# Kernel tuning notes

Measured on AMD Instinct MI355X. Metric: run time of the kernel, lower is better.

## Reference

```python
import jax, jax.numpy as jnp
import numpy as np
from jax import lax

B, T, F0 = 16, 1024, 128
L_CNN, L_RNN, D = 3, 3, 512
NF = F0 // 2  # 64, freq dim after stride-2 conv
EPS = 1e-5


def conv2d(x, w, b, stride, pad):
    # x: [B,C,H,W], w: [O,I,kh,kw]
    y = lax.conv_general_dilated(x, w, (stride, stride), [(pad, pad), (pad, pad)],
                                 dimension_numbers=('NCHW', 'OIHW', 'NCHW'))
    return y + b[None, :, None, None]


def ln_last(x, g, b):
    m = x.mean(-1, keepdims=True)
    v = ((x - m) ** 2).mean(-1, keepdims=True)
    return (x - m) * lax.rsqrt(v + EPS) * g + b


def ln_feats(x, g, b):
    # LayerNorm over freq axis (axis 2) of [B,C,F,T] (== transpose(2,3); LN; transpose back)
    m = x.mean(2, keepdims=True)
    v = ((x - m) ** 2).mean(2, keepdims=True)
    return (x - m) * lax.rsqrt(v + EPS) * g[None, None, :, None] + b[None, None, :, None]


def sru_dir(u, x_res, v, b, reverse):
    # u: [T,B,3,D] (candidate, f-pre, r-pre); x_res: [T,B,D] highway input; v,b: [2,D]
    u0 = u[:, :, 0]
    fp = u[:, :, 1] + b[0]
    rp = u[:, :, 2] + b[1]

    def step(c, inp):
        u0t, fpt, rpt, xrt = inp
        f = jax.nn.sigmoid(fpt + v[0] * c)
        r = jax.nn.sigmoid(rpt + v[1] * c)
        c = f * c + (1.0 - f) * u0t
        h = r * jnp.tanh(c) + (1.0 - r) * xrt
        return c, h

    c0 = jnp.zeros(u0.shape[1:], u.dtype)
    _, h = lax.scan(step, c0, (u0, fp, rp, x_res), reverse=reverse)
    return h  # [T,B,D]


def _forward(x, cnn_w, cnn_b, res_w1, res_b1, res_w2, res_b2,
             res_ln1_g, res_ln1_b, res_ln2_g, res_ln2_b,
             proj_w, sru_w, sru_v, sru_b, sru_ln_g, sru_ln_b,
             cls_ln_g, cls_ln_b, cls_w1, cls_b1, cls_w2, cls_b2):
    # stem conv: [B,1,128,1024] -> [B,32,64,512]
    x = conv2d(x, cnn_w, cnn_b, 2, 1)
    # residual CNN blocks (dropout = identity in eval)
    for i in range(L_CNN):
        res = x
        h = jax.nn.relu(ln_feats(x, res_ln1_g[i], res_ln1_b[i]))
        h = conv2d(h, res_w1[i], res_b1[i], 1, 1)
        h = jax.nn.relu(ln_feats(h, res_ln2_g[i], res_ln2_b[i]))
        h = conv2d(h, res_w2[i], res_b2[i], 1, 1)
        x = h + res
    # flatten channels x freq, time-major: [T', B, 32*NF]
    b_, c_, f_, t_ = x.shape
    x = x.reshape(b_, c_ * f_, t_).transpose(2, 0, 1)
    # proj_input_to_hidden_first: 2048 -> 2*D
    x = jnp.einsum('tbi,ih->tbh', x, proj_w)
    # bidirectional SRU layers
    for l in range(L_RNN):
        xl = ln_last(x, sru_ln_g[l], sru_ln_b[l])
        # u: [T,B,dir,gate,D]
        u = jnp.einsum('tbi,idkh->tbdkh', xl, sru_w[l])
        h_f = sru_dir(u[:, :, 0], x[..., :D], sru_v[l, 0], sru_b[l, 0], False)
        h_b = sru_dir(u[:, :, 1], x[..., D:], sru_v[l, 1], sru_b[l, 1], True)
        x = jnp.concatenate([h_f, h_b], axis=-1)
    # classifier: [B, T', 2D] -> [B, T', n_vocab+1]
    x = x.transpose(1, 0, 2)
    x = ln_last(x, cls_ln_g, cls_ln_b)
    x = jax.nn.relu(jnp.einsum('bth,hd->btd', x, cls_w1) + cls_b1)
    x = jnp.einsum('btd,dv->btv', x, cls_w2) + cls_b2
    return x


def setup_inputs() -> dict:
    key = jax.random.key(0)
    ks = iter(jax.random.split(key, 40))

    def rn(shape, s=0.05):
        return jax.random.normal(next(ks), shape, jnp.float32) * s

    return dict(
        x=jax.random.normal(next(ks), (B, 1, F0, T), jnp.float32),
        cnn_w=rn((32, 1, 3, 3)), cnn_b=jnp.zeros(32, jnp.float32),
        res_w1=rn((L_CNN, 32, 32, 3, 3)), res_b1=jnp.zeros((L_CNN, 32), jnp.float32),
        res_w2=rn((L_CNN, 32, 32, 3, 3)), res_b2=jnp.zeros((L_CNN, 32), jnp.float32),
        res_ln1_g=jnp.ones((L_CNN, NF), jnp.float32), res_ln1_b=jnp.zeros((L_CNN, NF), jnp.float32),
        res_ln2_g=jnp.ones((L_CNN, NF), jnp.float32), res_ln2_b=jnp.zeros((L_CNN, NF), jnp.float32),
        proj_w=rn((NF * 32, 2 * D), 0.02),
        sru_w=rn((L_RNN, 2 * D, 2, 3, D), 0.02),
        sru_v=rn((L_RNN, 2, 2, D), 0.1),
        sru_b=jnp.zeros((L_RNN, 2, 2, D), jnp.float32),
        sru_ln_g=jnp.ones((L_RNN, 2 * D), jnp.float32), sru_ln_b=jnp.zeros((L_RNN, 2 * D), jnp.float32),
        cls_ln_g=jnp.ones(2 * D, jnp.float32), cls_ln_b=jnp.zeros(2 * D, jnp.float32),
        cls_w1=rn((2 * D, D), 0.02), cls_b1=jnp.zeros(D, jnp.float32),
        cls_w2=rn((D, 29), 0.02), cls_b2=jnp.zeros(29, jnp.float32),
    )


def reference(x, cnn_w, cnn_b, res_w1, res_b1, res_w2, res_b2,
              res_ln1_g, res_ln1_b, res_ln2_g, res_ln2_b,
              proj_w, sru_w, sru_v, sru_b, sru_ln_g, sru_ln_b,
              cls_ln_g, cls_ln_b, cls_w1, cls_b1, cls_w2, cls_b2):
    return _forward(x, cnn_w, cnn_b, res_w1, res_b1, res_w2, res_b2,
                    res_ln1_g, res_ln1_b, res_ln2_g, res_ln2_b,
                    proj_w, sru_w, sru_v, sru_b, sru_ln_g, sru_ln_b,
                    cls_ln_g, cls_ln_b, cls_w1, cls_b1, cls_w2, cls_b2)
```

## Files before the change

### kernel.cpp

```cpp
#include <hip/hip_runtime.h>

typedef unsigned short u16;
typedef unsigned int u32;
typedef __attribute__((ext_vector_type(8))) short short8;
typedef __attribute__((ext_vector_type(4))) float floatx4;

__device__ __forceinline__ float bf2f(u16 u) {
    union { unsigned int i; float f; } v; v.i = ((unsigned int)u) << 16; return v.f;
}
__device__ __forceinline__ u16 f2bf(float f) {
    union { float f; unsigned int i; } v; v.f = f;
    unsigned int i = v.i + 0x7fffu + ((v.i >> 16) & 1u);
    return (u16)(i >> 16);
}

#define GLL(g, l) __builtin_amdgcn_global_load_lds( \
    (const __attribute__((address_space(1))) void*)(g), \
    (__attribute__((address_space(3))) void*)(l), 16, 0, 0)

#define WAITVM(n) asm volatile("s_waitcnt vmcnt(" #n ")" ::: "memory")
#define SBAR() __builtin_amdgcn_sched_barrier(0)

#define HA_BSTRIDE 1085568

__global__ __launch_bounds__(256) void sniff_k(const u16* __restrict__ x, int* __restrict__ flag) {
    __shared__ int red[4];
    int cnt = 0;
    for (int i = 0; i < 16; ++i) {
        u16 v = x[(threadIdx.x * 16 + i) * 2];
        int e = (v >> 7) & 0xFF;
        if (e >= 110 && e <= 135) cnt++;
    }
    #pragma unroll
    for (int off = 32; off; off >>= 1) cnt += __shfl_down(cnt, off);
    if ((threadIdx.x & 63) == 0) red[threadIdx.x >> 6] = cnt;
    __syncthreads();
    if (threadIdx.x == 0) {
        int tot = red[0] + red[1] + red[2] + red[3];
        *flag = (tot < 2048) ? 1 : 0;
    }
}

__device__ __forceinline__ float ldin(const void* p, size_t i, int isf32) {
    return isf32 ? ((const float*)p)[i] : bf2f(((const u16*)p)[i]);
}

struct CvtArgs {
    const void* src[19];
    int len[19];
    int off[19];
};
__global__ __launch_bounds__(256) void cvtall_k(CvtArgs a, float* __restrict__ dst,
                                                const int* __restrict__ flag) {
    int isf32 = *flag;
    int seg = blockIdx.y;
    int n = a.len[seg];
    const void* s = a.src[seg];
    float* d = dst + a.off[seg];
    for (int i = blockIdx.x * 256 + threadIdx.x; i < n; i += gridDim.x * 256)
        d[i] = ldin(s, i, isf32);
}

__global__ __launch_bounds__(256) void wtr_k(const void* __restrict__ W, int ldw, size_t wofs,
                                             u16* __restrict__ Wt, int ldt,
                                             const int* __restrict__ flag) {
    int isf32 = *flag;
    __shared__ u16 t[64][65];
    int k0 = blockIdx.x * 64, n0 = blockIdx.y * 64;
    int tid = threadIdx.x;
    #pragma unroll
    for (int i = 0; i < 16; ++i) {
        int kk = i * 4 + (tid >> 6), nn = tid & 63;
        t[kk][nn] = f2bf(ldin(W, wofs + (size_t)(k0 + kk) * ldw + n0 + nn, isf32));
    }
    __syncthreads();
    #pragma unroll
    for (int i = 0; i < 16; ++i) {
        int nn = i * 4 + (tid >> 6), kk = tid & 63;
        Wt[(size_t)(n0 + nn) * ldt + k0 + kk] = t[kk][nn];
    }
}

__global__ __launch_bounds__(256) void zero_k(float4* __restrict__ p, int n4) {
    float4 z = {0.f, 0.f, 0.f, 0.f};
    for (int i = blockIdx.x * 256 + threadIdx.x; i < n4; i += gridDim.x * 256) p[i] = z;
}
__global__ __launch_bounds__(256) void fill_k(float* __restrict__ p, int n) {
    int i = blockIdx.x * 256 + threadIdx.x;
    if (i < n) p[i] = 1.0e6f;
}

__global__ __launch_bounds__(256) void conv1_k(const void* __restrict__ x, const float* __restrict__ w,
                                               const float* __restrict__ bias, float* __restrict__ out,
                                               const int* __restrict__ flag) {
    int isf32 = *flag;
    int idx = blockIdx.x * 256 + threadIdx.x;
    int t  = idx & 511;
    int f  = (idx >> 9) & 63;
    int cg = (idx >> 15) & 7;
    int b  = idx >> 18;
    size_t xb = (size_t)b * 128 * 1024;

    float wr[4][9];
    #pragma unroll
    for (int i = 0; i < 4; ++i)
        #pragma unroll
        for (int k = 0; k < 9; ++k) wr[i][k] = w[(cg * 4 + i) * 9 + k];

    float acc[4];
    #pragma unroll
    for (int i = 0; i < 4; ++i) acc[i] = bias[cg * 4 + i];

    #pragma unroll
    for (int df = 0; df < 3; ++df) {
        int fi = 2 * f + df - 1;
        if (fi < 0 || fi >= 128) continue;
        size_t rowb = xb + (size_t)fi * 1024;
        float xv[3];
        #pragma unroll
        for (int dt = 0; dt < 3; ++dt) {
            int ti = 2 * t + dt - 1;
            float v = 0.f;
            if (ti >= 0 && ti < 1024) v = ldin(x, rowb + ti, isf32);
            xv[dt] = v;
        }
        #pragma unroll
        for (int i = 0; i < 4; ++i)
            #pragma unroll
            for (int dt = 0; dt < 3; ++dt)
                acc[i] = fmaf(wr[i][df * 3 + dt], xv[dt], acc[i]);
    }
    size_t obase = (((size_t)b * 32 + cg * 4) * 64 + f) * 512 + t;
    #pragma unroll
    for (int i = 0; i < 4; ++i) out[obase + (size_t)i * 64 * 512] = acc[i];
}

__global__ __launch_bounds__(256) void stats_k(const void* __restrict__ X, int isbf,
                                               float* __restrict__ sm, float* __restrict__ sr) {
    int idx = blockIdx.x * 256 + threadIdx.x;
    int t  = idx & 511;
    int bc = idx >> 9;
    size_t base = (size_t)bc * 64 * 512 + t;
    float s = 0.f, s2 = 0.f;
    #pragma unroll 8
    for (int f = 0; f < 64; ++f) {
        float v = isbf ? bf2f(((const u16*)X)[base + f * 512]) : ((const float*)X)[base + f * 512];
        s += v; s2 += v * v;
    }
    float m  = s * (1.f / 64.f);
    float var = fmaxf(s2 * (1.f / 64.f) - m * m, 0.f);
    sm[idx] = m;
    sr[idx] = rsqrtf(var + 1e-5f);
}

__global__ __launch_bounds__(256) void apply_k(const void* __restrict__ in, int isbf,
                                               const float* __restrict__ sm, const float* __restrict__ sr,
                                               const float* __restrict__ g, const float* __restrict__ be,
                                               u16* __restrict__ Ha) {
    int f = blockIdx.x;
    int b = blockIdx.y;
    float gg = g[f], bb_ = be[f];
    for (int it = 0; it < 2; ++it) {
        int t = it * 256 + threadIdx.x;
        u32 pk[16];
        #pragma unroll
        for (int cp = 0; cp < 16; ++cp) {
            u32 w = 0;
            #pragma unroll
            for (int half = 0; half < 2; ++half) {
                int ci = cp * 2 + half;
                size_t xi = (((size_t)b * 32 + ci) * 64 + f) * 512 + t;
                float xv = isbf ? bf2f(((const u16*)in)[xi]) : ((const float*)in)[xi];
                int si = (b * 32 + ci) * 512 + t;
                float hv = fmaxf((xv - sm[si]) * sr[si] * gg + bb_, 0.f);
                w |= ((u32)f2bf(hv)) << (half * 16);
            }
            pk[cp] = w;
        }
        u32* orow = (u32*)(Ha + (size_t)b * HA_BSTRIDE + ((size_t)(f + 1) * 514 + (t + 1)) * 32);
        #pragma unroll
        for (int q = 0; q < 16; ++q) orow[q] = pk[q];
    }
}

#define CVL 4
__global__ __launch_bounds__(256) void convm_k(const u16* __restrict__ Ha, void* __restrict__ out,
                                               const float* __restrict__ w, const float* __restrict__ bias,
                                               const float* __restrict__ res) {
    __shared__ __align__(16) u16 act[2][1536 * 8];
    int F0    = blockIdx.x * 16;
    int tbase = blockIdx.y * 64;
    int b     = blockIdx.z;
    const u16* Hb = Ha + (size_t)b * HA_BSTRIDE;
    int tid  = threadIdx.x;
    int lane = tid & 63;
    int wv   = tid >> 6;
    int quad = lane >> 4;
    int r    = lane & 15;
    int hasres = (res != nullptr);

    int ufp[6], utp[6], uq[6];
    #pragma unroll
    for (int it = 0; it < 6; ++it) {
        int u = it * 256 + tid;
        int u2 = (u < 1296) ? u : (u - 1296);
        int fp = u2 / 72;
        int rem = u2 - fp * 72;
        ufp[it] = fp; utp[it] = rem >> 2; uq[it] = rem & 3;
    }

    auto stage = [&](int tile, int bw) {
        int t00 = tbase + tile * 16;
        #pragma unroll
        for (int it = 0; it < 6; ++it) {
            int u = it * 256 + tid;
            GLL(Hb + ((size_t)(F0 + ufp[it]) * 514 + (t00 + utp[it])) * 32 + uq[it] * 8,
                &act[bw][u * 8]);
        }
    };

    short8 bfrag[3][3][2];
    #pragma unroll
    for (int df = 0; df < 3; ++df)
        #pragma unroll
        for (int dt = 0; dt < 3; ++dt)
            #pragma unroll
            for (int ct = 0; ct < 2; ++ct) {
                short8 v;
                #pragma unroll
                for (int j = 0; j < 8; ++j) {
                    int co = ct * 16 + r, ci = quad * 8 + j;
                    v[j] = (short)f2bf(w[(co * 32 + ci) * 9 + df * 3 + dt]);
                }
                bfrag[df][dt][ct] = v;
            }

    WAITVM(0);
    SBAR();
    stage(0, 0);
    SBAR();

    int fb = wv * 4;
    #pragma unroll 1
    for (int i = 0; i < CVL; ++i) {
        if (i < CVL - 1) stage(i + 1, (i + 1) & 1);
        SBAR();
        if (i == 0)            { WAITVM(6); }
        else if (i < CVL - 1)  { if (hasres) WAITVM(22); else WAITVM(14); }
        else                   { if (hasres) WAITVM(16); else WAITVM(8); }
        SBAR();
        __builtin_amdgcn_s_barrier();
        SBAR();

        const u16* ab = act[i & 1];
        floatx4 acc[4][2];
        #pragma unroll
        for (int ii = 0; ii < 4; ++ii)
            #pragma unroll
            for (int j = 0; j < 2; ++j)
                #pragma unroll
                for (int k = 0; k < 4; ++k) acc[ii][j][k] = 0.f;

        #pragma unroll
        for (int fh = 0; fh < 6; ++fh) {
            short8 af[3];
            #pragma unroll
            for (int dt = 0; dt < 3; ++dt)
                af[dt] = *(const short8*)&ab[((fb + fh) * 18 + (r + dt)) * 32 + quad * 8];
            #pragma unroll
            for (int df = 0; df < 3; ++df) {
                int rel = fh - df;
                if (rel < 0 || rel >= 4) continue;
                #pragma unroll
                for (int dt = 0; dt < 3; ++dt)
                    #pragma unroll
                    for (int ct = 0; ct < 2; ++ct)
                        acc[rel][ct] = __builtin_amdgcn_mfma_f32_16x16x32_bf16(
                            af[dt], bfrag[df][dt][ct], acc[rel][ct], 0, 0, 0);
            }
        }

        int t0 = tbase + i * 16;
        int tt = t0 + quad * 4;
        #pragma unroll
        for (int rel = 0; rel < 4; ++rel)
            #pragma unroll
            for (int ct = 0; ct < 2; ++ct) {
                int f  = F0 + fb + rel;
                int co = ct * 16 + r;
                size_t base = (((size_t)b * 32 + co) * 64 + f) * 512 + tt;
                float bs = bias[co];
                if (hasres) {
                    float4 rv = *(const float4*)(res + base);
                    float4 o;
                    o.x = acc[rel][ct][0] + bs + rv.x;
                    o.y = acc[rel][ct][1] + bs + rv.y;
                    o.z = acc[rel][ct][2] + bs + rv.z;
                    o.w = acc[rel][ct][3] + bs + rv.w;
                    *(float4*)((float*)out + base) = o;
                } else {
                    ushort4 o;
                    o.x = f2bf(acc[rel][ct][0] + bs);
                    o.y = f2bf(acc[rel][ct][1] + bs);
                    o.z = f2bf(acc[rel][ct][2] + bs);
                    o.w = f2bf(acc[rel][ct][3] + bs);
                    *(ushort4*)((u16*)out + base) = o;
                }
            }
        SBAR();
        __builtin_amdgcn_s_barrier();
        SBAR();
    }
}

__global__ __launch_bounds__(256) void transpose_k(const float* __restrict__ X, u16* __restrict__ A) {
    __shared__ float tile[64][65];
    int t0 = blockIdx.x * 64;
    int c  = blockIdx.y;
    int b  = blockIdx.z;
    const float* p = X + (((size_t)b * 32 + c) * 64) * 512 + t0;
    #pragma unroll
    for (int i = 0; i < 16; ++i) {
        int f = i * 4 + (threadIdx.x >> 6);
        int t = threadIdx.x & 63;
        tile[f][t] = p[(size_t)f * 512 + t];
    }
    __syncthreads();
    #pragma unroll
    for (int i = 0; i < 16; ++i) {
        int t = i * 4 + (threadIdx.x >> 6);
        int f = threadIdx.x & 63;
        A[((size_t)(t0 + t) * 16 + b) * 2048 + c * 64 + f] = f2bf(tile[f][t]);
    }
}

__global__ __launch_bounds__(256) void lnlast_k(const float* __restrict__ X, u16* __restrict__ Y,
                                                const float* __restrict__ g, const float* __restrict__ bt,
                                                int width) {
    int row = blockIdx.x;
    const float* p = X + (size_t)row * width;
    float s = 0.f, s2 = 0.f;
    for (int i = threadIdx.x; i < width; i += 256) { float v = p[i]; s += v; s2 += v * v; }
    #pragma unroll
    for (int off = 32; off; off >>= 1) { s += __shfl_down(s, off); s2 += __shfl_down(s2, off); }
    __shared__ float red[4][2];
    int wv = threadIdx.x >> 6;
    if ((threadIdx.x & 63) == 0) { red[wv][0] = s; red[wv][1] = s2; }
    __syncthreads();
    if (threadIdx.x == 0) {
        float a = 0.f, b2 = 0.f;
        for (int i = 0; i < 4; ++i) { a += red[i][0]; b2 += red[i][1]; }
        float m = a / width;
        float var = fmaxf(b2 / width - m * m, 0.f);
        red[0][0] = m; red[0][1] = rsqrtf(var + 1e-5f);
    }
    __syncthreads();
    float m = red[0][0], rs = red[0][1];
    u16* q = Y + (size_t)row * width;
    for (int i = threadIdx.x; i < width; i += 256)
        q[i] = f2bf((p[i] - m) * rs * g[i] + bt[i]);
}

__global__ __launch_bounds__(256) void gemm_bt(const u16* __restrict__ A, const u16* __restrict__ A2,
                                               int lda, const u16* __restrict__ Bt, int ldb,
                                               void* __restrict__ C, void* __restrict__ C2,
                                               int ldc, int nsplit,
                                               const float* __restrict__ bias, int relu, int K,
                                               int obf) {
    __shared__ __align__(16) u16 As[3][128 * 32];
    __shared__ __align__(16) u16 Bs[3][128 * 32];
    int tid  = threadIdx.x;
    int bm   = blockIdx.x * 128;
    int bn   = blockIdx.y * 128;

    const u16* Ab = A;
    void* Cb = C;
    int cn = bn;
    if (bn >= nsplit) { Ab = A2; Cb = C2; cn = bn - nsplit; }

    int lane = tid & 63;
    int wv   = tid >> 6;
    int quad = lane >> 4;
    int r    = lane & 15;
    int wm   = (wv >> 1) * 64;
    int wn   = (wv & 1) * 64;

    floatx4 acc[4][4];
    #pragma unroll
    for (int i = 0; i < 4; ++i)
        #pragma unroll
        for (int j = 0; j < 4; ++j)
            #pragma unroll
            for (int k = 0; k < 4; ++k) acc[i][j][k] = 0.f;

    int row0 = tid >> 2;
    int ks0  = ((tid & 3) ^ ((tid >> 3) & 3)) * 8;
    const u16* Ab1 = Ab + (size_t)(bm + row0) * lda + ks0;
    const u16* Ab2 = Ab + (size_t)(bm + 64 + row0) * lda + ks0;
    const u16* Bb1 = Bt + (size_t)(bn + row0) * ldb + ks0;
    const u16* Bb2 = Bt + (size_t)(bn + 64 + row0) * ldb + ks0;

    auto stage = [&](int ks, int bw) {
        int k0 = ks * 32;
        GLL(Ab1 + k0, &As[bw][tid * 8]);
        GLL(Ab2 + k0, &As[bw][2048 + tid * 8]);
        GLL(Bb1 + k0, &Bs[bw][tid * 8]);
        GLL(Bb2 + k0, &Bs[bw][2048 + tid * 8]);
    };

    int nk = K >> 5;
    WAITVM(0);
    SBAR();
    stage(0, 0); stage(1, 1); stage(2, 2);
    SBAR();

    int col = (quad ^ ((r >> 1) & 3)) * 8;
    int bc = 0;
    #pragma unroll 1
    for (int i = 0; i < nk; ++i) {
        if (i + 2 < nk)       { WAITVM(8); }
        else if (i + 1 < nk)  { WAITVM(4); }
        else                  { WAITVM(0); }
        SBAR();
        __builtin_amdgcn_s_barrier();
        SBAR();

        const u16* as = As[bc];
        const u16* bs = Bs[bc];
        short8 af[4], bf[4];
        #pragma unroll
        for (int mi = 0; mi < 4; ++mi) af[mi] = *(const short8*)&as[(wm + mi * 16 + r) * 32 + col];
        #pragma unroll
        for (int ni = 0; ni < 4; ++ni) bf[ni] = *(const short8*)&bs[(wn + ni * 16 + r) * 32 + col];
        #pragma unroll
        for (int mi = 0; mi < 4; ++mi)
            #pragma unroll
            for (int ni = 0; ni < 4; ++ni)
                acc[mi][ni] = __builtin_amdgcn_mfma_f32_16x16x32_bf16(af[mi], bf[ni], acc[mi][ni], 0, 0, 0);

        SBAR();
        __builtin_amdgcn_s_barrier();
        SBAR();
        if (i + 3 < nk) stage(i + 3, bc);
        bc = (bc == 2) ? 0 : bc + 1;
    }

    #pragma unroll
    for (int mi = 0; mi < 4; ++mi)
        #pragma unroll
        for (int ni = 0; ni < 4; ++ni) {
            int ccol = cn + wn + ni * 16 + r;
            float bsv = bias ? bias[ccol] : 0.f;
            #pragma unroll
            for (int reg = 0; reg < 4; ++reg) {
                int row = bm + wm + mi * 16 + quad * 4 + reg;
                float v = acc[mi][ni][reg] + bsv;
                if (relu) v = fmaxf(v, 0.f);
                if (obf) ((u16*)Cb)[(size_t)row * ldc + ccol] = f2bf(v);
                else     ((float*)Cb)[(size_t)row * ldc + ccol] = v;
            }
        }
}

#define TC 256
__global__ __launch_bounds__(64) void scan_k(const u16* __restrict__ Uf, const u16* __restrict__ Ub,
                                             const float* __restrict__ Xp, float* __restrict__ Xn,
                                             float* __restrict__ cstate, const float* __restrict__ vv,
                                             const float* __restrict__ bb, int t0f, int t0b, int init) {
    __shared__ __align__(16) char lds[4][10240];
    int tid = threadIdx.x;
    int d   = blockIdx.x >> 7;
    int idx = blockIdx.x & 127;
    int b   = idx >> 3;
    int h0  = (idx & 7) * 64;
    int h   = h0 + tid;
    int gid = d * 8192 + idx * 64 + tid;

    float v0 = vv[(d * 2 + 0) * 512 + h];
    float v1 = vv[(d * 2 + 1) * 512 + h];
    float b0 = bb[(d * 2 + 0) * 512 + h];
    float b1 = bb[(d * 2 + 1) * 512 + h];
    const u16* U = d ? Ub : Uf;
    int t0 = d ? t0b : t0f;
    float* ob = Xn + (size_t)b * 1024 + d * 512 + h;
    float cc = init ? 0.f : cstate[gid];
    int tstp = d ? -16384 : 16384;

    const char* gp[10];
    int dlt[10];
    #pragma unroll
    for (int it = 0; it < 10; ++it) {
        int u = it * 64 + tid;
        int s = u / 40;
        int j = u - s * 40;
        int sl0 = d ? (TC - 1 - s) : s;
        if (j < 24) {
            int k = j >> 3, jj = j & 7;
            gp[it] = (const char*)(U + ((size_t)(sl0 * 16 + b) * 1536 + k * 512 + h0 + jj * 8));
            dlt[it] = d ? -786432 : 786432;
        } else {
            gp[it] = (const char*)(Xp + ((size_t)(t0 + sl0) * 16384 + (size_t)b * 1024 + d * 512 + h0 + (j - 24) * 4));
            dlt[it] = d ? -1048576 : 1048576;
        }
    }
    char* lbase = (char*)&lds[0][0] + tid * 16;
    auto stage = [&](int bw) {
        char* lb = lbase + bw * 10240;
        #pragma unroll
        for (int it = 0; it < 10; ++it) {
            GLL(gp[it], lb + it * 1024);
            gp[it] += dlt[it];
        }
    };

    asm volatile("s_waitcnt vmcnt(0)" ::: "memory");
    SBAR();
    stage(0);
    stage(1);
    stage(2);
    SBAR();

    #pragma unroll 1
    for (int tk = 0; tk < 16; ++tk) {
        switch (tk) {
            case 0:  WAITVM(20); break;
            case 1:  WAITVM(36); break;
            case 14: WAITVM(42); break;
            case 15: WAITVM(32); break;
            default: WAITVM(52); break;
        }
        SBAR();
        const char* Bb = (const char*)&lds[0][0] + (size_t)(tk & 3) * 10240;
        float* op = ob + (size_t)(t0 + (d ? (TC - 1 - tk * 16) : tk * 16)) * 16384;
        #pragma unroll
        for (int s = 0; s < 16; ++s) {
            const char* sb = Bb + s * 640;
            float u0 = bf2f(*(const u16*)(sb + tid * 2));
            float fp = bf2f(*(const u16*)(sb + 128 + tid * 2)) + b0;
            float rp = bf2f(*(const u16*)(sb + 256 + tid * 2)) + b1;
            float xr = *(const float*)(sb + 384 + tid * 4);
            float f = 1.f / (1.f + __expf(-(fp + v0 * cc)));
            float r = 1.f / (1.f + __expf(-(rp + v1 * cc)));
            cc = f * cc + (1.f - f) * u0;
            float th = 1.f - 2.f / (__expf(2.f * cc) + 1.f);
            *op = r * th + (1.f - r) * xr;
            op += tstp;
        }
        SBAR();
        if (tk < 13) stage((tk + 3) & 3);
        SBAR();
    }
    cstate[gid] = cc;
}

__global__ __launch_bounds__(256) void cls2_k(const float* __restrict__ FC1, const float* __restrict__ W2,
                                              const float* __restrict__ b2, void* __restrict__ out,
                                              const int* __restrict__ flag) {
    int isf32 = *flag;
    int tid = threadIdx.x;
    int rh = tid >> 7;
    int ks = (tid >> 5) & 3;
    int v  = tid & 31;
    int row = blockIdx.x * 2 + rh;
    const float* p = FC1 + (size_t)row * 512 + ks * 128;
    const float* wp = W2 + (size_t)ks * 128 * 29;
    float acc = 0.f;
    #pragma unroll 4
    for (int k = 0; k < 128; ++k) {
        float wv = (v < 29) ? wp[k * 29 + v] : 0.f;
        acc = fmaf(p[k], wv, acc);
    }
    acc += __shfl_xor(acc, 32);
    __shared__ float red[2][2][32];
    if ((tid & 63) < 32) red[rh][(tid >> 6) & 1][v] = acc;
    __syncthreads();
    if ((tid & 127) < 32 && v < 29) {
        float s = red[rh][0][v] + red[rh][1][v] + b2[v];
        int t = row >> 4, b = row & 15;
        size_t oi = ((size_t)b * 512 + t) * 29 + v;
        if (isf32) ((float*)out)[oi] = s;
        else       ((u16*)out)[oi]   = f2bf(s);
    }
}

extern "C" void kernel_launch(void* const* d_in, const int* in_sizes, int n_in,
                              void* d_out, int out_size, void* d_ws, size_t ws_size,
                              hipStream_t stream) {
    const void* x      = d_in[0];
    const void* proj_w = d_in[11];
    const void* sru_w  = d_in[12];
    const void* cls_w1 = d_in[19];

    float* ws = (float*)d_ws;
    const size_t O_X    = 0;
    const size_t O_C    = 16777216;
    const size_t O_HA   = 25165824;
    const size_t O_SM   = 33850368;
    const size_t O_SR   = 34112512;
    const size_t O_CST  = 34374656;
    const size_t O_PARK = 34391040;
    const size_t O_FLAG = 34483488;
    const size_t TOTAL  = 34483504;
    if (ws_size < TOTAL * sizeof(float)) {
        fill_k<<<(out_size + 255) / 256, 256, 0, stream>>>((float*)d_out, out_size);
        return;
    }

    float* X   = ws + O_X;
    u16*   C   = (u16*)(ws + O_C);
    u16*   HA  = (u16*)(ws + O_HA);
    float* SM  = ws + O_SM;
    float* SR  = ws + O_SR;
    float* CST = ws + O_CST;
    float* PK  = ws + O_PARK;
    int*   FLG = (int*)(ws + O_FLAG);

    u16*   Abf = (u16*)(ws + O_C);
    u16*   BtP = (u16*)(ws + 0);
    float* XP0 = ws + 25165824;
    u16*   XL  = (u16*)(ws + 0);
    float* XP1 = ws + 4194304;
    u16*   Uf  = (u16*)(ws + 12582912);
    u16*   Ub  = (u16*)(ws + 15728640);
    u16*   BtS = (u16*)(ws + 18874368);
    u16*   BtC = (u16*)(ws + O_SM);
    float* FC1 = ws + 12582912;

    float* p_cnn_w = PK + 0;      float* p_cnn_b = PK + 288;
    float* p_rw1   = PK + 320;    float* p_rb1   = PK + 27968;
    float* p_rw2   = PK + 28064;  float* p_rb2   = PK + 55712;
    float* p_l1g   = PK + 55808;  float* p_l1b   = PK + 56000;
    float* p_l2g   = PK + 56192;  float* p_l2b   = PK + 56384;
    float* p_sv    = PK + 56576;  float* p_sb    = PK + 62720;
    float* p_slng  = PK + 68864;  float* p_slnb  = PK + 71936;
    float* p_clng  = PK + 75008;  float* p_clnb  = PK + 76032;
    float* p_cb1   = PK + 77056;  float* p_cw2   = PK + 77568;
    float* p_cb2   = PK + 92416;

    sniff_k<<<1, 256, 0, stream>>>((const u16*)x, FLG);

    CvtArgs ca;
    const int srcidx[19] = {1,2,3,4,5,6,7,8,9,10,13,14,15,16,17,18,20,21,22};
    const int lens[19]   = {288,32,27648,96,27648,96,192,192,192,192,6144,6144,3072,3072,1024,1024,512,14848,29};
    const int offs[19]   = {0,288,320,27968,28064,55712,55808,56000,56192,56384,56576,62720,68864,71936,75008,76032,77056,77568,92416};
    for (int i = 0; i < 19; ++i) { ca.src[i] = d_in[srcidx[i]]; ca.len[i] = lens[i]; ca.off[i] = offs[i]; }
    cvtall_k<<<dim3(108, 19), 256, 0, stream>>>(ca, PK, FLG);

    zero_k<<<2048, 256, 0, stream>>>((float4*)HA, 2171136);
    conv1_k<<<16384, 256, 0, stream>>>(x, p_cnn_w, p_cnn_b, X, FLG);

    for (int i = 0; i < 3; ++i) {
        stats_k<<<1024, 256, 0, stream>>>(X, 0, SM, SR);
        apply_k<<<dim3(64, 16), 256, 0, stream>>>(X, 0, SM, SR, p_l1g + i * 64, p_l1b + i * 64, HA);
        convm_k<<<dim3(4, 8, 16), 256, 0, stream>>>(HA, C, p_rw1 + i * 9216, p_rb1 + i * 32, nullptr);
        stats_k<<<1024, 256, 0, stream>>>(C, 1, SM, SR);
        apply_k<<<dim3(64, 16), 256, 0, stream>>>(C, 1, SM, SR, p_l2g + i * 64, p_l2b + i * 64, HA);
        convm_k<<<dim3(4, 8, 16), 256, 0, stream>>>(HA, X, p_rw2 + i * 9216, p_rb2 + i * 32, X);
    }

    transpose_k<<<dim3(8, 32, 16), 256, 0, stream>>>(X, Abf);
    wtr_k<<<dim3(32, 16), 256, 0, stream>>>(proj_w, 1024, 0, BtP, 2048, FLG);
    gemm_bt<<<dim3(64, 8), 256, 0, stream>>>(Abf, Abf, 2048, BtP, 2048, XP0, XP0, 1024,
                                             1 << 30, nullptr, 0, 2048, 0);

    for (int l = 0; l < 3; ++l)
        wtr_k<<<dim3(16, 48), 256, 0, stream>>>(sru_w, 3072, (size_t)l * 3145728,
                                                BtS + (size_t)l * 3145728, 1024, FLG);
    wtr_k<<<dim3(16, 8), 256, 0, stream>>>(cls_w1, 512, 0, BtC, 1024, FLG);

    float* cur = XP0;
    float* nxt = XP1;
    for (int l = 0; l < 3; ++l) {
        lnlast_k<<<8192, 256, 0, stream>>>(cur, XL, p_slng + l * 1024, p_slnb + l * 1024, 1024);
        const u16* Btl = BtS + (size_t)l * 3145728;
        for (int j = 0; j < 2; ++j) {
            int t0f = j * TC;
            int t0b = (1 - j) * TC;
            gemm_bt<<<dim3(32, 24), 256, 0, stream>>>(XL + (size_t)t0f * 16 * 1024,
                                                      XL + (size_t)t0b * 16 * 1024, 1024,
                                                      Btl, 1024, Uf, Ub, 1536, 1536,
                                                      nullptr, 0, 1024, 1);
            scan_k<<<256, 64, 0, stream>>>(Uf, Ub, cur, nxt, CST,
                                           p_sv + l * 2048, p_sb + l * 2048, t0f, t0b, j == 0);
        }
        float* tmp = cur; cur = nxt; nxt = tmp;
    }

    lnlast_k<<<8192, 256, 0, stream>>>(cur, XL, p_clng, p_clnb, 1024);
    gemm_bt<<<dim3(64, 4), 256, 0, stream>>>(XL, XL, 1024, BtC, 1024, FC1, FC1, 512,
                                             1 << 30, p_cb1, 1, 1024, 0);
    cls2_k<<<4096, 256, 0, stream>>>(FC1, p_cw2, p_cb2, d_out, FLG);
}
```

Before: 1.399 ms.

## Fuse LayerNorm statistics into conv epilogue via atomic partial sums

The residual conv kernel now accumulates per-(batch, channel, time) sums and sums of squares of its outputs. It reduces them across waves in shared memory and adds them into global buffers with atomics. A small finalize kernel turns these sums into mean and rsqrt-variance, replacing the separate stats pass that reread the full activation tensor before each LayerNorm apply. This removes five full-tensor reads. In exchange it adds zeroing and finalize launches, global atomics, an extra block barrier per tile, and retuned vmcnt waits. For the bf16 path the statistics now come from pre-rounding fp32 values.

```diff
diff --git a/kernel.cpp b/kernel.cpp
--- a/kernel.cpp
+++ b/kernel.cpp
@@ -19,6 +19,7 @@
     (__attribute__((address_space(3))) void*)(l), 16, 0, 0)
 
 #define WAITVM(n) asm volatile("s_waitcnt vmcnt(" #n ")" ::: "memory")
+#define WAITLG() asm volatile("s_waitcnt lgkmcnt(0)" ::: "memory")
 #define SBAR() __builtin_amdgcn_sched_barrier(0)
 
 #define HA_BSTRIDE 1085568
@@ -147,10 +148,17 @@
         float v = isbf ? bf2f(((const u16*)X)[base + f * 512]) : ((const float*)X)[base + f * 512];
         s += v; s2 += v * v;
     }
-    float m  = s * (1.f / 64.f);
+    sm[idx] = s;
+    sr[idx] = s2;
+}
+
+__global__ __launch_bounds__(256) void finalize_k(float* __restrict__ sm, float* __restrict__ sr) {
+    int i = blockIdx.x * 256 + threadIdx.x;
+    float s = sm[i], s2 = sr[i];
+    float m = s * (1.f / 64.f);
     float var = fmaxf(s2 * (1.f / 64.f) - m * m, 0.f);
-    sm[idx] = m;
-    sr[idx] = rsqrtf(var + 1e-5f);
+    sm[i] = m;
+    sr[i] = rsqrtf(var + 1e-5f);
 }
 
 __global__ __launch_bounds__(256) void apply_k(const void* __restrict__ in, int isbf,
@@ -186,8 +194,11 @@
 #define CVL 4
 __global__ __launch_bounds__(256) void convm_k(const u16* __restrict__ Ha, void* __restrict__ out,
                                                const float* __restrict__ w, const float* __restrict__ bias,
-                                               const float* __restrict__ res) {
+                                               const float* __restrict__ res,
+                                               float* __restrict__ smx, float* __restrict__ srx) {
     __shared__ __align__(16) u16 act[2][1536 * 8];
+    __shared__ float ssS[4][32][17];
+    __shared__ float ssQ[4][32][17];
     int F0    = blockIdx.x * 16;
     int tbase = blockIdx.y * 64;
     int b     = blockIdx.z;
@@ -197,7 +208,8 @@
     int wv   = tid >> 6;
     int quad = lane >> 4;
     int r    = lane & 15;
-    int hasres = (res != nullptr);
+    int hasres  = (res != nullptr);
+    int dostats = (smx != nullptr);
 
     int ufp[6], utp[6], uq[6];
     #pragma unroll
@@ -245,9 +257,14 @@
     for (int i = 0; i < CVL; ++i) {
         if (i < CVL - 1) stage(i + 1, (i + 1) & 1);
         SBAR();
-        if (i == 0)            { WAITVM(6); }
-        else if (i < CVL - 1)  { if (hasres) WAITVM(22); else WAITVM(14); }
-        else                   { if (hasres) WAITVM(16); else WAITVM(8); }
+        if (i == 0)           { WAITVM(6); }
+        else if (i < CVL - 1) {
+            if (hasres) { if (dostats) WAITVM(26); else WAITVM(22); }
+            else        { if (dostats) WAITVM(18); else WAITVM(14); }
+        } else {
+            if (hasres) { if (dostats) WAITVM(20); else WAITVM(16); }
+            else        { if (dostats) WAITVM(12); else WAITVM(8); }
+        }
         SBAR();
         __builtin_amdgcn_s_barrier();
         SBAR();
@@ -282,6 +299,12 @@
 
         int t0 = tbase + i * 16;
         int tt = t0 + quad * 4;
+        float ps[2][4], p2s[2][4];
+        #pragma unroll
+        for (int ct = 0; ct < 2; ++ct)
+            #pragma unroll
+            for (int rg = 0; rg < 4; ++rg) { ps[ct][rg] = 0.f; p2s[ct][rg] = 0.f; }
+
         #pragma unroll
         for (int rel = 0; rel < 4; ++rel)
             #pragma unroll
@@ -290,23 +313,57 @@
                 int co = ct * 16 + r;
                 size_t base = (((size_t)b * 32 + co) * 64 + f) * 512 + tt;
                 float bs = bias[co];
+                float v4[4];
                 if (hasres) {
                     float4 rv = *(const float4*)(res + base);
-                    float4 o;
-                    o.x = acc[rel][ct][0] + bs + rv.x;
-                    o.y = acc[rel][ct][1] + bs + rv.y;
-                    o.z = acc[rel][ct][2] + bs + rv.z;
-                    o.w = acc[rel][ct][3] + bs + rv.w;
+                    v4[0] = acc[rel][ct][0] + bs + rv.x;
+                    v4[1] = acc[rel][ct][1] + bs + rv.y;
+                    v4[2] = acc[rel][ct][2] + bs + rv.z;
+                    v4[3] = acc[rel][ct][3] + bs + rv.w;
+                    float4 o = {v4[0], v4[1], v4[2], v4[3]};
                     *(float4*)((float*)out + base) = o;
                 } else {
+                    v4[0] = acc[rel][ct][0] + bs;
+                    v4[1] = acc[rel][ct][1] + bs;
+                    v4[2] = acc[rel][ct][2] + bs;
+                    v4[3] = acc[rel][ct][3] + bs;
                     ushort4 o;
-                    o.x = f2bf(acc[rel][ct][0] + bs);
-                    o.y = f2bf(acc[rel][ct][1] + bs);
-                    o.z = f2bf(acc[rel][ct][2] + bs);
-                    o.w = f2bf(acc[rel][ct][3] + bs);
+                    o.x = f2bf(v4[0]); o.y = f2bf(v4[1]);
+                    o.z = f2bf(v4[2]); o.w = f2bf(v4[3]);
                     *(ushort4*)((u16*)out + base) = o;
                 }
+                #pragma unroll
+                for (int rg = 0; rg < 4; ++rg) {
+                    ps[ct][rg]  += v4[rg];
+                    p2s[ct][rg] += v4[rg] * v4[rg];
+                }
             }
+
+        if (dostats) {
+            #pragma unroll
+            for (int ct = 0; ct < 2; ++ct)
+                #pragma unroll
+                for (int rg = 0; rg < 4; ++rg) {
+                    int co = ct * 16 + r;
+                    int j  = quad * 4 + rg;
+                    ssS[wv][co][j] = ps[ct][rg];
+                    ssQ[wv][co][j] = p2s[ct][rg];
+                }
+            WAITLG();
+            SBAR();
+            __builtin_amdgcn_s_barrier();
+            SBAR();
+            #pragma unroll
+            for (int s_ = 0; s_ < 2; ++s_) {
+                int slot = s_ * 256 + tid;
+                int co = slot >> 4, j = slot & 15;
+                float a = ssS[0][co][j] + ssS[1][co][j] + ssS[2][co][j] + ssS[3][co][j];
+                float q = ssQ[0][co][j] + ssQ[1][co][j] + ssQ[2][co][j] + ssQ[3][co][j];
+                int gi = ((b * 32 + co) << 9) + t0 + j;
+                atomicAdd(&smx[gi], a);
+                atomicAdd(&srx[gi], q);
+            }
+        }
         SBAR();
         __builtin_amdgcn_s_barrier();
         SBAR();
@@ -649,13 +706,23 @@
     zero_k<<<2048, 256, 0, stream>>>((float4*)HA, 2171136);
     conv1_k<<<16384, 256, 0, stream>>>(x, p_cnn_w, p_cnn_b, X, FLG);
 
+    stats_k<<<1024, 256, 0, stream>>>(X, 0, SM, SR);
     for (int i = 0; i < 3; ++i) {
-        stats_k<<<1024, 256, 0, stream>>>(X, 0, SM, SR);
+        finalize_k<<<1024, 256, 0, stream>>>(SM, SR);
         apply_k<<<dim3(64, 16), 256, 0, stream>>>(X, 0, SM, SR, p_l1g + i * 64, p_l1b + i * 64, HA);
-        convm_k<<<dim3(4, 8, 16), 256, 0, stream>>>(HA, C, p_rw1 + i * 9216, p_rb1 + i * 32, nullptr);
-        stats_k<<<1024, 256, 0, stream>>>(C, 1, SM, SR);
+        zero_k<<<512, 256, 0, stream>>>((float4*)SM, 131072);
+        convm_k<<<dim3(4, 8, 16), 256, 0, stream>>>(HA, C, p_rw1 + i * 9216, p_rb1 + i * 32,
+                                                    nullptr, SM, SR);
+        finalize_k<<<1024, 256, 0, stream>>>(SM, SR);
         apply_k<<<dim3(64, 16), 256, 0, stream>>>(C, 1, SM, SR, p_l2g + i * 64, p_l2b + i * 64, HA);
-        convm_k<<<dim3(4, 8, 16), 256, 0, stream>>>(HA, X, p_rw2 + i * 9216, p_rb2 + i * 32, X);
+        if (i < 2) {
+            zero_k<<<512, 256, 0, stream>>>((float4*)SM, 131072);
+            convm_k<<<dim3(4, 8, 16), 256, 0, stream>>>(HA, X, p_rw2 + i * 9216, p_rb2 + i * 32,
+                                                        X, SM, SR);
+        } else {
+            convm_k<<<dim3(4, 8, 16), 256, 0, stream>>>(HA, X, p_rw2 + i * 9216, p_rb2 + i * 32,
+                                                        X, nullptr, nullptr);
+        }
     }
 
     transpose_k<<<dim3(8, 32, 16), 256, 0, stream>>>(X, Abf);
```

Result: faster. 1.365 ms (-2.4%).
